# Performance work log

Hardware: AMD Instinct MI355X
Metric: run time of the kernel (lower is better)

The kernel has to match this reference:

```python
import jax, jax.numpy as jnp
import numpy as np

B, S, E, H, N = 16384, 256, 128, 128, 34  # batch, state_dim, reduced_lang_dim, mlp hidden, N_task
TEMP = 0.1
EPS = 1e-8  # torch cosine_similarity eps


def setup_inputs() -> dict:
    key = jax.random.key(0)
    ks = jax.random.split(key, 12)
    sc = 0.05
    return {
        "state": jax.random.normal(ks[0], (B, S), dtype=jnp.float32),
        "task_id": jax.random.randint(ks[1], (B,), 0, N),
        "prior": jax.random.normal(ks[2], (B, N), dtype=jnp.float32),
        # stacked weights of the 34 per-task MLPs (Linear(S,H) -> ReLU -> Linear(H,H) -> ReLU -> Linear(H,E))
        "W1": jax.random.normal(ks[3], (N, S, H), dtype=jnp.float32) * sc,
        "b1": jax.random.normal(ks[4], (N, H), dtype=jnp.float32) * sc,
        "W2": jax.random.normal(ks[5], (N, H, H), dtype=jnp.float32) * sc,
        "b2": jax.random.normal(ks[6], (N, H), dtype=jnp.float32) * sc,
        "W3": jax.random.normal(ks[7], (N, H, E), dtype=jnp.float32) * sc,
        "b3": jax.random.normal(ks[8], (N, E), dtype=jnp.float32) * sc,
        "lang_emb": jax.random.normal(ks[9], (N, E), dtype=jnp.float32),
    }


def reference(state, task_id, prior, W1, b1, W2, b2, W3, b3, lang_emb):
    # 34 parallel MLPs as a single batched GEMM stack: [B,S] x [N,S,H] -> [B,N,H]
    h = jax.nn.relu(jnp.einsum('bs,nsh->bnh', state, W1) + b1)
    h = jax.nn.relu(jnp.einsum('bnh,nhk->bnk', h, W2) + b2)
    q = jnp.einsum('bnk,nke->bne', h, W3) + b3            # [B,N,E]
    # normalize (torch.norm division, no eps, then cosine_similarity renormalizes -> unit)
    q = q / jnp.linalg.norm(q, axis=-1, keepdims=True)
    lang = lang_emb[task_id]                              # [B,E]
    lang_n = lang / jnp.maximum(jnp.linalg.norm(lang, axis=-1, keepdims=True), EPS)
    cos_sim = jnp.einsum('bne,be->bn', q, lang_n)         # [B,N]
    log_task_prob = jax.nn.log_softmax(cos_sim / TEMP, axis=-1)
    task_prob_prior = jax.nn.softmax(prior, axis=-1)      # exp(log_softmax(prior))
    latent_vec = jnp.einsum('bne,bn->be', q, task_prob_prior)
    latent_target = jax.lax.stop_gradient(q[jnp.arange(B), task_id])  # detach
    rep_vec = jnp.concatenate([state, latent_vec], axis=-1)           # [B, S+E]
    return rep_vec, log_task_prob, latent_target, latent_vec
```

## Files before the change

### kernel.cpp

```cpp
#include <hip/hip_runtime.h>
#include <hip/hip_bf16.h>
#include <hip/hip_fp16.h>
#include <cstdint>
#include <cstddef>

typedef __bf16 bf16;
typedef __attribute__((ext_vector_type(8))) __bf16 bf16x8;
typedef __attribute__((ext_vector_type(16))) float f32x16;

static_assert(sizeof(bf16x8) == 16, "bf16x8 must be 16B");

#define NTASK 34
#define BTOT 16384
#define WSTRIDE 73728

__device__ __forceinline__ f32x16 mfma32(bf16x8 a, bf16x8 b, f32x16 c) {
  return __builtin_amdgcn_mfma_f32_32x32x16_bf16(a, b, c, 0, 0, 0);
}

__device__ __forceinline__ void gload_lds16(const void* g, void* l) {
  __builtin_amdgcn_global_load_lds((__attribute__((address_space(1))) void*)g,
                                   (__attribute__((address_space(3))) void*)l,
                                   16, 0, 0);
}

__device__ __forceinline__ unsigned pack2(float lo, float hi) {
  union { __bf16 h[2]; unsigned u; } v;
  v.h[0] = (__bf16)lo; v.h[1] = (__bf16)hi;
  return v.u;
}

__device__ __forceinline__ void pl32swap(unsigned &a, unsigned &b) {
  asm volatile("v_permlane32_swap_b32 %0, %1" : "+v"(a), "+v"(b));
}

__global__ void prep_all(const float* __restrict__ W1, const float* __restrict__ W2,
                         const float* __restrict__ W3, const float* __restrict__ b1,
                         const float* __restrict__ b2, const float* __restrict__ b3,
                         const float* __restrict__ state, const float* __restrict__ prior,
                         bf16* __restrict__ wdst, bf16* __restrict__ sdst,
                         float* __restrict__ ppt) {
  int bid = blockIdx.x;
  if (bid < 1190) {
    int idx = bid * 256 + threadIdx.x;
    if (idx >= 304640) return;
    int n = idx / (140 * 64);
    int r = idx - n * (140 * 64);
    int bb = r >> 6, l = r & 63;
    const float *W, *bias; int real, mt, ks, Kt;
    size_t off;
    if (bb < 68)       { W = W1; bias = b1; mt = bb / 17; ks = bb - mt * 17; real = 16; Kt = 256;
                         off = (size_t)bb * 512; }
    else if (bb < 104) { W = W2; bias = b2; int t = bb - 68;  mt = t / 9; ks = t - mt * 9; real = 8; Kt = 128;
                         off = 36864 + (size_t)(bb - 68) * 512; }
    else               { W = W3; bias = b3; int t = bb - 104; mt = t / 9; ks = t - mt * 9; real = 8; Kt = 128;
                         off = 36864 + 18432 + (size_t)(bb - 104) * 512; }
    int col = mt * 32 + (l & 31);
    bf16x8 v;
    if (ks < real) {
      int k0 = ks * 16 + ((l >> 5) << 3);
      const float* s = W + ((size_t)n * Kt + k0) * 128 + col;
#pragma unroll
      for (int j = 0; j < 8; ++j) v[j] = (bf16)s[(size_t)j * 128];
    } else {
#pragma unroll
      for (int j = 0; j < 8; ++j) v[j] = (bf16)0.f;
      if (l < 32) v[0] = (bf16)bias[n * 128 + col];
    }
    *(bf16x8*)(wdst + (size_t)n * WSTRIDE + off + l * 8) = v;
  } else if (bid < 3238) {
    int idx = (bid - 1190) * 256 + threadIdx.x;
    int rb = idx >> 10;
    int r = idx & 1023;
    int ks = r >> 6;
    int l = r & 63;
    int b = rb * 32 + (l & 31);
    int k0 = ks * 16 + ((l >> 5) << 3);
    const float* s = state + (size_t)b * 256 + k0;
    bf16x8 v;
#pragma unroll
    for (int j = 0; j < 8; ++j) v[j] = (bf16)s[j];
    *(bf16x8*)(sdst + (size_t)(rb * 16 + ks) * 512 + l * 8) = v;
  } else {
    int row = (bid - 3238) * 4 + (threadIdx.x >> 6);
    int lane = threadIdx.x & 63;
    float v = (lane < NTASK) ? prior[(size_t)row * NTASK + lane] : -INFINITY;
    float m = v;
#pragma unroll
    for (int mm = 1; mm < 64; mm <<= 1) m = fmaxf(m, __shfl_xor(m, mm));
    float e = (lane < NTASK) ? expf(v - m) : 0.0f;
    float s = e;
#pragma unroll
    for (int mm = 1; mm < 64; mm <<= 1) s += __shfl_xor(s, mm);
    if (lane < NTASK) ppt[(size_t)lane * BTOT + row] = e / s;
  }
}

__global__ void prep_langn(const float* __restrict__ lang, float* __restrict__ out) {
  __shared__ float red[2];
  int n = blockIdx.x;
  int t = threadIdx.x;
  float v = lang[(size_t)n * 128 + t];
  float ss = v * v;
#pragma unroll
  for (int m = 1; m < 64; m <<= 1) ss += __shfl_xor(ss, m);
  if ((t & 63) == 0) red[t >> 6] = ss;
  __syncthreads();
  float s = red[0] + red[1];
  float sc = 1.0f / fmaxf(sqrtf(s), 1e-8f);
  out[(size_t)n * 128 + t] = v * sc;
}


__global__ void __launch_bounds__(256, 2)
pass1_kernel(const int* __restrict__ task_id, const bf16* __restrict__ wstream,
             const bf16* __restrict__ sf, const float* __restrict__ langn,
             const float* __restrict__ pp_t,
             float* __restrict__ cs_t, __half* __restrict__ lat_part,
             float* __restrict__ out_tgt) {
  __shared__ __align__(16) bf16 shW[36864];

  const int tid = threadIdx.x;
  const int l = tid & 63;
  const int w = tid >> 6;
  const int hi = l >> 5;
  const int b = l & 31;
  const int tg = blockIdx.x >> 7;
  const int rg = blockIdx.x & 127;
  const int start = tg * 4 + (tg < 2 ? tg : 2);
  const int cnt = 4 + (tg < 2 ? 1 : 0);
  const int row0 = rg * 128 + w * 32 + b;
  const int rb0 = rg * 4 + w;

  int tidn0 = task_id[row0];

  {
    const bf16* wb0 = wstream + (size_t)start * WSTRIDE;
#pragma unroll
    for (int c = 0; c < 17; ++c)
      gload_lds16(wb0 + c * 2048 + tid * 8, shW + c * 2048 + tid * 8);
  }

  union { unsigned u[4]; bf16x8 v; } cf;
  cf.u[0] = (l < 32) ? 0x3f80u : 0u;
  cf.u[1] = 0u; cf.u[2] = 0u; cf.u[3] = 0u;

  f32x16 z;
#pragma unroll
  for (int i = 0; i < 16; ++i) z[i] = 0.f;
  f32x16 lat[4] = {z, z, z, z};

  const bf16* sb0 = sf + (size_t)rb0 * 8192 + l * 8;

  auto transition = [&](f32x16* acc, bf16x8* f) {
#pragma unroll
    for (int mt = 0; mt < 4; ++mt) {
      unsigned p[8];
#pragma unroll
      for (int q = 0; q < 4; ++q) {
        p[2 * q]     = pack2(fmaxf(acc[mt][4 * q + 0], 0.f), fmaxf(acc[mt][4 * q + 1], 0.f));
        p[2 * q + 1] = pack2(fmaxf(acc[mt][4 * q + 2], 0.f), fmaxf(acc[mt][4 * q + 3], 0.f));
      }
      pl32swap(p[0], p[2]); pl32swap(p[1], p[3]);
      pl32swap(p[4], p[6]); pl32swap(p[5], p[7]);
      union { unsigned u[4]; bf16x8 v; } e, o;
      e.u[0] = p[0]; e.u[1] = p[1]; e.u[2] = p[2]; e.u[3] = p[3];
      o.u[0] = p[4]; o.u[1] = p[5]; o.u[2] = p[6]; o.u[3] = p[7];
      f[2 * mt] = e.v; f[2 * mt + 1] = o.v;
    }
  };

  for (int t = 0; t < cnt; ++t) {
    const int n = start + t;
    const bf16* wbase = wstream + (size_t)n * WSTRIDE;

    asm volatile("s_waitcnt vmcnt(0)" ::: "memory");
    __builtin_amdgcn_s_barrier();

    f32x16 acc[4] = {z, z, z, z};

    bf16x8 s0[4];
#pragma unroll
    for (int i = 0; i < 4; ++i) s0[i] = *(const bf16x8*)(sb0 + i * 512);
#pragma unroll
    for (int ks = 0; ks < 16; ++ks) {
      bf16x8 sv = s0[ks & 3];
      if (ks < 12) s0[ks & 3] = *(const bf16x8*)(sb0 + (ks + 4) * 512);
      __builtin_amdgcn_s_setprio(1);
#pragma unroll
      for (int mt = 0; mt < 4; ++mt) {
        bf16x8 wf = *(const bf16x8*)(shW + ((mt * 17 + ks) << 9) + l * 8);
        acc[mt] = mfma32(wf, sv, acc[mt]);
      }
      __builtin_amdgcn_s_setprio(0);
    }
#pragma unroll
    for (int mt = 0; mt < 4; ++mt) {
      bf16x8 wf = *(const bf16x8*)(shW + ((mt * 17 + 16) << 9) + l * 8);
      acc[mt] = mfma32(wf, cf.v, acc[mt]);
    }

    __builtin_amdgcn_s_barrier();

#pragma unroll
    for (int c = 0; c < 18; ++c)
      gload_lds16(wbase + 36864 + c * 2048 + tid * 8, shW + c * 2048 + tid * 8);

    bf16x8 f2[8];
    transition(acc, f2);

    asm volatile("s_waitcnt vmcnt(9)" ::: "memory");
    __builtin_amdgcn_s_barrier();

#pragma unroll
    for (int mt = 0; mt < 4; ++mt) acc[mt] = z;
#pragma unroll
    for (int ks = 0; ks < 8; ++ks) {
      __builtin_amdgcn_s_setprio(1);
#pragma unroll
      for (int mt = 0; mt < 4; ++mt) {
        bf16x8 wf = *(const bf16x8*)(shW + ((mt * 9 + ks) << 9) + l * 8);
        acc[mt] = mfma32(wf, f2[ks], acc[mt]);
      }
      __builtin_amdgcn_s_setprio(0);
    }
#pragma unroll
    for (int mt = 0; mt < 4; ++mt) {
      bf16x8 wf = *(const bf16x8*)(shW + ((mt * 9 + 8) << 9) + l * 8);
      acc[mt] = mfma32(wf, cf.v, acc[mt]);
    }

    bf16x8 f3[8];
    transition(acc, f3);

    asm volatile("s_waitcnt vmcnt(0)" ::: "memory");
    __builtin_amdgcn_s_barrier();

#pragma unroll
    for (int mt = 0; mt < 4; ++mt) acc[mt] = z;
#pragma unroll
    for (int ks = 0; ks < 8; ++ks) {
      __builtin_amdgcn_s_setprio(1);
#pragma unroll
      for (int mt = 0; mt < 4; ++mt) {
        bf16x8 wf = *(const bf16x8*)(shW + ((36 + mt * 9 + ks) << 9) + l * 8);
        acc[mt] = mfma32(wf, f3[ks], acc[mt]);
      }
      __builtin_amdgcn_s_setprio(0);
    }
#pragma unroll
    for (int mt = 0; mt < 4; ++mt) {
      bf16x8 wf = *(const bf16x8*)(shW + ((36 + mt * 9 + 8) << 9) + l * 8);
      acc[mt] = mfma32(wf, cf.v, acc[mt]);
    }

    __builtin_amdgcn_s_barrier();

    if (t + 1 < cnt) {
      const bf16* wnext = wstream + (size_t)(n + 1) * WSTRIDE;
#pragma unroll
      for (int c = 0; c < 17; ++c)
        gload_lds16(wnext + c * 2048 + tid * 8, shW + c * 2048 + tid * 8);
    }

    float ssq = 0.f, dot = 0.f;
    const float* lgb = langn + (size_t)tidn0 * 128;
#pragma unroll
    for (int mt = 0; mt < 4; ++mt)
#pragma unroll
      for (int q = 0; q < 4; ++q) {
        int c0 = mt * 32 + q * 8 + 4 * hi;
        float4 lg = *(const float4*)(lgb + c0);
        float a0 = acc[mt][4 * q + 0], a1 = acc[mt][4 * q + 1];
        float a2 = acc[mt][4 * q + 2], a3 = acc[mt][4 * q + 3];
        ssq += a0 * a0 + a1 * a1 + a2 * a2 + a3 * a3;
        dot += a0 * lg.x + a1 * lg.y + a2 * lg.z + a3 * lg.w;
      }
    ssq += __shfl_xor(ssq, 32);
    dot += __shfl_xor(dot, 32);
    float inv = rsqrtf(ssq);
    if (l < 32) cs_t[(size_t)row0 * NTASK + n] = dot * inv;
    float pwi = pp_t[(size_t)n * BTOT + row0] * inv;
#pragma unroll
    for (int mt = 0; mt < 4; ++mt) lat[mt] += acc[mt] * pwi;
    if (tidn0 == n) {
#pragma unroll
      for (int mt = 0; mt < 4; ++mt)
#pragma unroll
        for (int q = 0; q < 4; ++q) {
          float4 qv = {acc[mt][4 * q + 0] * inv, acc[mt][4 * q + 1] * inv,
                       acc[mt][4 * q + 2] * inv, acc[mt][4 * q + 3] * inv};
          *(float4*)(out_tgt + (size_t)row0 * 128 + mt * 32 + q * 8 + 4 * hi) = qv;
        }
    }
  }

  __half* lp = lat_part + ((size_t)tg * BTOT + row0) * 128;
#pragma unroll
  for (int mt = 0; mt < 4; ++mt)
#pragma unroll
    for (int q = 0; q < 4; ++q) {
      int c0 = mt * 32 + q * 8 + 4 * hi;
      union { __half h[4]; uint2 u; } v;
      v.h[0] = __float2half(lat[mt][4 * q + 0]);
      v.h[1] = __float2half(lat[mt][4 * q + 1]);
      v.h[2] = __float2half(lat[mt][4 * q + 2]);
      v.h[3] = __float2half(lat[mt][4 * q + 3]);
      *(uint2*)(lp + c0) = v.u;
    }
}


__global__ void __launch_bounds__(256)
pass3_kernel(const float* __restrict__ state, const float* __restrict__ cs_t,
             const __half* __restrict__ lat_part,
             float* __restrict__ out_rep, float* __restrict__ out_ltp,
             float* __restrict__ out_lat) {
  int w = threadIdx.x >> 6, l = threadIdx.x & 63;
  size_t row = (size_t)blockIdx.x * 4 + w;

  float c = (l < NTASK) ? cs_t[row * NTASK + l] * 10.0f : -1e30f;
  float cm = c;
#pragma unroll
  for (int mm = 1; mm < 64; mm <<= 1) cm = fmaxf(cm, __shfl_xor(cm, mm));
  float ce = (l < NTASK) ? expf(c - cm) : 0.0f;
  float cs = ce;
#pragma unroll
  for (int mm = 1; mm < 64; mm <<= 1) cs += __shfl_xor(cs, mm);
  if (l < NTASK) out_ltp[row * NTASK + l] = c - cm - logf(cs);

  float2 lv = {0.f, 0.f};
#pragma unroll
  for (int g = 0; g < 8; ++g) {
    __half2 p = *(const __half2*)(lat_part + ((size_t)g * BTOT + row) * 128 + 2 * l);
    lv.x += __low2float(p);
    lv.y += __high2float(p);
  }
  *(float2*)(out_lat + row * 128 + 2 * l) = lv;
  *(float2*)(out_rep + row * 384 + 256 + 2 * l) = lv;

  float4 sv = *(const float4*)(state + row * 256 + l * 4);
  *(float4*)(out_rep + row * 384 + l * 4) = sv;
}


extern "C" void kernel_launch(void* const* d_in, const int* in_sizes, int n_in,
                              void* d_out, int out_size, void* d_ws, size_t ws_size,
                              hipStream_t stream) {
  (void)in_sizes; (void)n_in; (void)out_size; (void)ws_size;
  const float* state = (const float*)d_in[0];
  const int* task_id = (const int*)d_in[1];
  const float* prior = (const float*)d_in[2];
  const float* W1 = (const float*)d_in[3];
  const float* b1 = (const float*)d_in[4];
  const float* W2 = (const float*)d_in[5];
  const float* b2 = (const float*)d_in[6];
  const float* W3 = (const float*)d_in[7];
  const float* b3 = (const float*)d_in[8];
  const float* lang = (const float*)d_in[9];

  char* ws = (char*)d_ws;
  bf16* wstream  = (bf16*)(ws + 0);
  bf16* sf       = (bf16*)(ws + 5013504);
  float* langn   = (float*)(ws + 13402112);
  float* pp_t    = (float*)(ws + 13419520);
  float* cs_t    = (float*)(ws + 15647744);
  __half* lat_part = (__half*)(ws + 17875968);

  float* out = (float*)d_out;
  float* out_rep = out;
  float* out_ltp = out + 6291456;
  float* out_tgt = out + 6848512;
  float* out_lat = out + 8945664;

  prep_all<<<7334, 256, 0, stream>>>(W1, W2, W3, b1, b2, b3, state, prior,
                                     wstream, sf, pp_t);
  prep_langn<<<NTASK, 128, 0, stream>>>(lang, langn);
  pass1_kernel<<<1024, 256, 0, stream>>>(task_id, wstream, sf, langn, pp_t,
                                         cs_t, lat_part, out_tgt);
  pass3_kernel<<<4096, 256, 0, stream>>>(state, cs_t, lat_part,
                                         out_rep, out_ltp, out_lat);
}
```

Before: 148.5 us.

## Double-buffer weight windows in LDS and regroup tasks into six groups

```diff
diff --git a/kernel.cpp b/kernel.cpp
--- a/kernel.cpp
+++ b/kernel.cpp
@@ -41,35 +41,41 @@
                          bf16* __restrict__ wdst, bf16* __restrict__ sdst,
                          float* __restrict__ ppt) {
   int bid = blockIdx.x;
-  if (bid < 1190) {
+  if (bid < 1224) {
     int idx = bid * 256 + threadIdx.x;
-    if (idx >= 304640) return;
-    int n = idx / (140 * 64);
-    int r = idx - n * (140 * 64);
-    int bb = r >> 6, l = r & 63;
-    const float *W, *bias; int real, mt, ks, Kt;
-    size_t off;
-    if (bb < 68)       { W = W1; bias = b1; mt = bb / 17; ks = bb - mt * 17; real = 16; Kt = 256;
-                         off = (size_t)bb * 512; }
-    else if (bb < 104) { W = W2; bias = b2; int t = bb - 68;  mt = t / 9; ks = t - mt * 9; real = 8; Kt = 128;
-                         off = 36864 + (size_t)(bb - 68) * 512; }
-    else               { W = W3; bias = b3; int t = bb - 104; mt = t / 9; ks = t - mt * 9; real = 8; Kt = 128;
-                         off = 36864 + 18432 + (size_t)(bb - 104) * 512; }
-    int col = mt * 32 + (l & 31);
+    int n = idx / 9216;
+    int r = idx - n * 9216;
+    int g = r >> 8;
+    int m = (r >> 6) & 3;
+    int l = r & 63;
+    int col = m * 32 + (l & 31);
+    int kj = (l >> 5) << 3;
     bf16x8 v;
-    if (ks < real) {
-      int k0 = ks * 16 + ((l >> 5) << 3);
-      const float* s = W + ((size_t)n * Kt + k0) * 128 + col;
+#pragma unroll
+    for (int j = 0; j < 8; ++j) v[j] = (bf16)0.f;
+    if (g < 16) {
+      const float* s = W1 + ((size_t)n * 256 + g * 16 + kj) * 128 + col;
+#pragma unroll
+      for (int j = 0; j < 8; ++j) v[j] = (bf16)s[(size_t)j * 128];
+    } else if (g == 16) {
+      if (l < 32) v[0] = (bf16)b1[n * 128 + col];
+    } else if (g == 17) {
+    } else if (g < 26) {
+      const float* s = W2 + ((size_t)n * 128 + (g - 18) * 16 + kj) * 128 + col;
+#pragma unroll
+      for (int j = 0; j < 8; ++j) v[j] = (bf16)s[(size_t)j * 128];
+    } else if (g == 26) {
+      if (l < 32) v[0] = (bf16)b2[n * 128 + col];
+    } else if (g < 35) {
+      const float* s = W3 + ((size_t)n * 128 + (g - 27) * 16 + kj) * 128 + col;
 #pragma unroll
       for (int j = 0; j < 8; ++j) v[j] = (bf16)s[(size_t)j * 128];
     } else {
-#pragma unroll
-      for (int j = 0; j < 8; ++j) v[j] = (bf16)0.f;
-      if (l < 32) v[0] = (bf16)bias[n * 128 + col];
-    }
-    *(bf16x8*)(wdst + (size_t)n * WSTRIDE + off + l * 8) = v;
-  } else if (bid < 3238) {
-    int idx = (bid - 1190) * 256 + threadIdx.x;
+      if (l < 32) v[0] = (bf16)b3[n * 128 + col];
+    }
+    *(bf16x8*)(wdst + (size_t)n * WSTRIDE + (size_t)(g * 4 + m) * 512 + l * 8) = v;
+  } else if (bid < 3272) {
+    int idx = (bid - 1224) * 256 + threadIdx.x;
     int rb = idx >> 10;
     int r = idx & 1023;
     int ks = r >> 6;
@@ -82,7 +88,7 @@
     for (int j = 0; j < 8; ++j) v[j] = (bf16)s[j];
     *(bf16x8*)(sdst + (size_t)(rb * 16 + ks) * 512 + l * 8) = v;
   } else {
-    int row = (bid - 3238) * 4 + (threadIdx.x >> 6);
+    int row = (bid - 3272) * 4 + (threadIdx.x >> 6);
     int lane = threadIdx.x & 63;
     float v = (lane < NTASK) ? prior[(size_t)row * NTASK + lane] : -INFINITY;
     float m = v;
@@ -112,34 +118,49 @@
 }
 
 
-__global__ void __launch_bounds__(256, 2)
+__global__ void __launch_bounds__(256, 3)
 pass1_kernel(const int* __restrict__ task_id, const bf16* __restrict__ wstream,
              const bf16* __restrict__ sf, const float* __restrict__ langn,
              const float* __restrict__ pp_t,
              float* __restrict__ cs_t, __half* __restrict__ lat_part,
              float* __restrict__ out_tgt) {
-  __shared__ __align__(16) bf16 shW[36864];
+  __shared__ __align__(16) bf16 shW[24576];
 
   const int tid = threadIdx.x;
   const int l = tid & 63;
-  const int w = tid >> 6;
+  const int wid = tid >> 6;
   const int hi = l >> 5;
   const int b = l & 31;
   const int tg = blockIdx.x >> 7;
   const int rg = blockIdx.x & 127;
-  const int start = tg * 4 + (tg < 2 ? tg : 2);
-  const int cnt = 4 + (tg < 2 ? 1 : 0);
-  const int row0 = rg * 128 + w * 32 + b;
-  const int rb0 = rg * 4 + w;
-
-  int tidn0 = task_id[row0];
-
-  {
-    const bf16* wb0 = wstream + (size_t)start * WSTRIDE;
-#pragma unroll
-    for (int c = 0; c < 17; ++c)
-      gload_lds16(wb0 + c * 2048 + tid * 8, shW + c * 2048 + tid * 8);
-  }
+  const int start = (tg < 4) ? tg * 6 : (24 + (tg - 4) * 5);
+  const int cnt = (tg < 4) ? 6 : 5;
+  const int row0 = rg * 128 + wid * 32 + b;
+  const int rb0 = rg * 4 + wid;
+
+  const int tidn = task_id[row0];
+  const bf16* sb = sf + (size_t)rb0 * 8192 + l * 8;
+
+#define STAGE_WIN(slot, srcoff) \
+  { _Pragma("unroll") \
+    for (int c = 0; c < 6; ++c) \
+      gload_lds16(wstream + (srcoff) + c * 2048 + tid * 8, \
+                  shW + (slot) * 12288 + c * 2048 + tid * 8); }
+
+#define WIN_TOP() \
+  { asm volatile("s_waitcnt vmcnt(0)" ::: "memory"); \
+    __builtin_amdgcn_s_barrier(); }
+
+#define KMFMA(slot, gl, bop) \
+  { _Pragma("unroll") \
+    for (int mt = 0; mt < 4; ++mt) { \
+      bf16x8 wf = *(const bf16x8*)(shW + (slot) * 12288 + ((gl) * 4 + mt) * 512 + l * 8); \
+      acc[mt] = mfma32(wf, (bop), acc[mt]); } }
+
+  STAGE_WIN(0, (size_t)start * WSTRIDE);
+  bf16x8 sring[4];
+#pragma unroll
+  for (int i = 0; i < 4; ++i) sring[i] = *(const bf16x8*)(sb + i * 512);
 
   union { unsigned u[4]; bf16x8 v; } cf;
   cf.u[0] = (l < 32) ? 0x3f80u : 0u;
@@ -148,9 +169,13 @@
   f32x16 z;
 #pragma unroll
   for (int i = 0; i < 16; ++i) z[i] = 0.f;
-  f32x16 lat[4] = {z, z, z, z};
-
-  const bf16* sb0 = sf + (size_t)rb0 * 8192 + l * 8;
+
+  const __half2 hz = __float2half2_rn(0.0f);
+  __half2 lat[4][4][2];
+#pragma unroll
+  for (int mt = 0; mt < 4; ++mt)
+#pragma unroll
+    for (int q = 0; q < 4; ++q) { lat[mt][q][0] = hz; lat[mt][q][1] = hz; }
 
   auto transition = [&](f32x16* acc, bf16x8* f) {
 #pragma unroll
@@ -172,99 +197,86 @@
 
   for (int t = 0; t < cnt; ++t) {
     const int n = start + t;
-    const bf16* wbase = wstream + (size_t)n * WSTRIDE;
-
-    asm volatile("s_waitcnt vmcnt(0)" ::: "memory");
-    __builtin_amdgcn_s_barrier();
-
-    f32x16 acc[4] = {z, z, z, z};
-
-    bf16x8 s0[4];
-#pragma unroll
-    for (int i = 0; i < 4; ++i) s0[i] = *(const bf16x8*)(sb0 + i * 512);
-#pragma unroll
-    for (int ks = 0; ks < 16; ++ks) {
-      bf16x8 sv = s0[ks & 3];
-      if (ks < 12) s0[ks & 3] = *(const bf16x8*)(sb0 + (ks + 4) * 512);
-      __builtin_amdgcn_s_setprio(1);
-#pragma unroll
-      for (int mt = 0; mt < 4; ++mt) {
-        bf16x8 wf = *(const bf16x8*)(shW + ((mt * 17 + ks) << 9) + l * 8);
-        acc[mt] = mfma32(wf, sv, acc[mt]);
-      }
-      __builtin_amdgcn_s_setprio(0);
-    }
-#pragma unroll
-    for (int mt = 0; mt < 4; ++mt) {
-      bf16x8 wf = *(const bf16x8*)(shW + ((mt * 17 + 16) << 9) + l * 8);
-      acc[mt] = mfma32(wf, cf.v, acc[mt]);
-    }
-
-    __builtin_amdgcn_s_barrier();
-
-#pragma unroll
-    for (int c = 0; c < 18; ++c)
-      gload_lds16(wbase + 36864 + c * 2048 + tid * 8, shW + c * 2048 + tid * 8);
-
-    bf16x8 f2[8];
+    const size_t wb = (size_t)n * WSTRIDE;
+    f32x16 acc[4];
+    bf16x8 f2[8], f3[8];
+
+    WIN_TOP();
+    STAGE_WIN(1, wb + 12288);
+#pragma unroll
+    for (int mt = 0; mt < 4; ++mt) acc[mt] = z;
+    __builtin_amdgcn_s_setprio(1);
+#pragma unroll
+    for (int gl = 0; gl < 6; ++gl) {
+      bf16x8 sv = sring[gl & 3];
+      sring[gl & 3] = *(const bf16x8*)(sb + (gl + 4) * 512);
+      KMFMA(0, gl, sv);
+    }
+    __builtin_amdgcn_s_setprio(0);
+
+    WIN_TOP();
+    STAGE_WIN(0, wb + 24576);
+    __builtin_amdgcn_s_setprio(1);
+#pragma unroll
+    for (int gl = 0; gl < 6; ++gl) {
+      int ks = 6 + gl;
+      bf16x8 sv = sring[ks & 3];
+      sring[ks & 3] = *(const bf16x8*)(sb + (ks + 4) * 512);
+      KMFMA(1, gl, sv);
+    }
+    __builtin_amdgcn_s_setprio(0);
+
+    WIN_TOP();
+    STAGE_WIN(1, wb + 36864);
+    __builtin_amdgcn_s_setprio(1);
+#pragma unroll
+    for (int gl = 0; gl < 4; ++gl) {
+      int ks = 12 + gl;
+      KMFMA(0, gl, sring[ks & 3]);
+    }
+    KMFMA(0, 4, cf.v);
+    __builtin_amdgcn_s_setprio(0);
     transition(acc, f2);
 
-    asm volatile("s_waitcnt vmcnt(9)" ::: "memory");
-    __builtin_amdgcn_s_barrier();
-
+    WIN_TOP();
+    STAGE_WIN(0, wb + 49152);
 #pragma unroll
     for (int mt = 0; mt < 4; ++mt) acc[mt] = z;
-#pragma unroll
-    for (int ks = 0; ks < 8; ++ks) {
-      __builtin_amdgcn_s_setprio(1);
-#pragma unroll
-      for (int mt = 0; mt < 4; ++mt) {
-        bf16x8 wf = *(const bf16x8*)(shW + ((mt * 9 + ks) << 9) + l * 8);
-        acc[mt] = mfma32(wf, f2[ks], acc[mt]);
-      }
-      __builtin_amdgcn_s_setprio(0);
-    }
-#pragma unroll
-    for (int mt = 0; mt < 4; ++mt) {
-      bf16x8 wf = *(const bf16x8*)(shW + ((mt * 9 + 8) << 9) + l * 8);
-      acc[mt] = mfma32(wf, cf.v, acc[mt]);
-    }
-
-    bf16x8 f3[8];
+    __builtin_amdgcn_s_setprio(1);
+#pragma unroll
+    for (int gl = 0; gl < 6; ++gl) KMFMA(1, gl, f2[gl]);
+    __builtin_amdgcn_s_setprio(0);
+
+    WIN_TOP();
+    STAGE_WIN(1, wb + 61440);
+    __builtin_amdgcn_s_setprio(1);
+    KMFMA(0, 0, f2[6]);
+    KMFMA(0, 1, f2[7]);
+    KMFMA(0, 2, cf.v);
+    __builtin_amdgcn_s_setprio(0);
     transition(acc, f3);
-
-    asm volatile("s_waitcnt vmcnt(0)" ::: "memory");
-    __builtin_amdgcn_s_barrier();
-
 #pragma unroll
     for (int mt = 0; mt < 4; ++mt) acc[mt] = z;
-#pragma unroll
-    for (int ks = 0; ks < 8; ++ks) {
-      __builtin_amdgcn_s_setprio(1);
-#pragma unroll
-      for (int mt = 0; mt < 4; ++mt) {
-        bf16x8 wf = *(const bf16x8*)(shW + ((36 + mt * 9 + ks) << 9) + l * 8);
-        acc[mt] = mfma32(wf, f3[ks], acc[mt]);
-      }
-      __builtin_amdgcn_s_setprio(0);
-    }
-#pragma unroll
-    for (int mt = 0; mt < 4; ++mt) {
-      bf16x8 wf = *(const bf16x8*)(shW + ((36 + mt * 9 + 8) << 9) + l * 8);
-      acc[mt] = mfma32(wf, cf.v, acc[mt]);
-    }
-
-    __builtin_amdgcn_s_barrier();
-
+    __builtin_amdgcn_s_setprio(1);
+    KMFMA(0, 3, f3[0]);
+    KMFMA(0, 4, f3[1]);
+    KMFMA(0, 5, f3[2]);
+    __builtin_amdgcn_s_setprio(0);
+
+    WIN_TOP();
     if (t + 1 < cnt) {
-      const bf16* wnext = wstream + (size_t)(n + 1) * WSTRIDE;
-#pragma unroll
-      for (int c = 0; c < 17; ++c)
-        gload_lds16(wnext + c * 2048 + tid * 8, shW + c * 2048 + tid * 8);
-    }
+      STAGE_WIN(0, wb + WSTRIDE);
+#pragma unroll
+      for (int i = 0; i < 4; ++i) sring[i] = *(const bf16x8*)(sb + i * 512);
+    }
+    __builtin_amdgcn_s_setprio(1);
+#pragma unroll
+    for (int gl = 0; gl < 5; ++gl) KMFMA(1, gl, f3[3 + gl]);
+    KMFMA(1, 5, cf.v);
+    __builtin_amdgcn_s_setprio(0);
 
     float ssq = 0.f, dot = 0.f;
-    const float* lgb = langn + (size_t)tidn0 * 128;
+    const float* lgb = langn + (size_t)tidn * 128;
 #pragma unroll
     for (int mt = 0; mt < 4; ++mt)
 #pragma unroll
@@ -281,9 +293,17 @@
     float inv = rsqrtf(ssq);
     if (l < 32) cs_t[(size_t)row0 * NTASK + n] = dot * inv;
     float pwi = pp_t[(size_t)n * BTOT + row0] * inv;
-#pragma unroll
-    for (int mt = 0; mt < 4; ++mt) lat[mt] += acc[mt] * pwi;
-    if (tidn0 == n) {
+    __half2 pw2 = __float2half2_rn(pwi);
+#pragma unroll
+    for (int mt = 0; mt < 4; ++mt)
+#pragma unroll
+      for (int q = 0; q < 4; ++q) {
+        lat[mt][q][0] = __hfma2(__floats2half2_rn(acc[mt][4 * q + 0], acc[mt][4 * q + 1]),
+                                pw2, lat[mt][q][0]);
+        lat[mt][q][1] = __hfma2(__floats2half2_rn(acc[mt][4 * q + 2], acc[mt][4 * q + 3]),
+                                pw2, lat[mt][q][1]);
+      }
+    if (tidn == n) {
 #pragma unroll
       for (int mt = 0; mt < 4; ++mt)
 #pragma unroll
@@ -301,13 +321,14 @@
 #pragma unroll
     for (int q = 0; q < 4; ++q) {
       int c0 = mt * 32 + q * 8 + 4 * hi;
-      union { __half h[4]; uint2 u; } v;
-      v.h[0] = __float2half(lat[mt][4 * q + 0]);
-      v.h[1] = __float2half(lat[mt][4 * q + 1]);
-      v.h[2] = __float2half(lat[mt][4 * q + 2]);
-      v.h[3] = __float2half(lat[mt][4 * q + 3]);
+      union { __half2 h[2]; uint2 u; } v;
+      v.h[0] = lat[mt][q][0];
+      v.h[1] = lat[mt][q][1];
       *(uint2*)(lp + c0) = v.u;
     }
+#undef STAGE_WIN
+#undef WIN_TOP
+#undef KMFMA
 }
 
 
@@ -331,7 +352,7 @@
 
   float2 lv = {0.f, 0.f};
 #pragma unroll
-  for (int g = 0; g < 8; ++g) {
+  for (int g = 0; g < 6; ++g) {
     __half2 p = *(const __half2*)(lat_part + ((size_t)g * BTOT + row) * 128 + 2 * l);
     lv.x += __low2float(p);
     lv.y += __high2float(p);
@@ -373,11 +394,11 @@
   float* out_tgt = out + 6848512;
   float* out_lat = out + 8945664;
 
-  prep_all<<<7334, 256, 0, stream>>>(W1, W2, W3, b1, b2, b3, state, prior,
+  prep_all<<<7368, 256, 0, stream>>>(W1, W2, W3, b1, b2, b3, state, prior,
                                      wstream, sf, pp_t);
   prep_langn<<<NTASK, 128, 0, stream>>>(lang, langn);
-  pass1_kernel<<<1024, 256, 0, stream>>>(task_id, wstream, sf, langn, pp_t,
-                                         cs_t, lat_part, out_tgt);
+  pass1_kernel<<<768, 256, 0, stream>>>(task_id, wstream, sf, langn, pp_t,
+                                        cs_t, lat_part, out_tgt);
   pass3_kernel<<<4096, 256, 0, stream>>>(state, cs_t, lat_part,
                                          out_rep, out_ltp, out_lat);
 }
```

New measurement: 166.1 us. 1.12x slower.
